# Optimization experiments

Hardware: AMD Instinct MI355X
Metric: run time of the kernel (lower is better)

The kernel has to match this reference:

```python
import jax, jax.numpy as jnp
import numpy as np

S = 14
B = 2
C = 20
LAMBDA_COORD = 5.0
LAMBDA_NOOBJ = 0.5
BATCH = 4096


def setup_inputs() -> dict:
    key = jax.random.key(0)
    k1, k2, k3 = jax.random.split(key, 3)
    pred = jax.random.uniform(k1, (BATCH, S, S, B * 5 + C), dtype=jnp.float32)
    target = jax.random.uniform(k2, (BATCH, S, S, B * 5 + C), dtype=jnp.float32)
    obj = (jax.random.uniform(k3, (BATCH, S, S), dtype=jnp.float32) < 0.15).astype(jnp.float32)
    target = target.at[..., 4].set(obj)
    target = target.at[..., 9].set(obj)
    return {"pred": pred, "target": target}


def _iou(box1, box2):
    # box1, box2: (..., 4) = [x, y, w, h]; elementwise IoU over leading dims
    b1x1 = box1[..., 0] - box1[..., 2] / 2
    b1y1 = box1[..., 1] - box1[..., 3] / 2
    b1x2 = box1[..., 0] + box1[..., 2] / 2
    b1y2 = box1[..., 1] + box1[..., 3] / 2
    b2x1 = box2[..., 0] - box2[..., 2] / 2
    b2y1 = box2[..., 1] - box2[..., 3] / 2
    b2x2 = box2[..., 0] + box2[..., 2] / 2
    b2y2 = box2[..., 1] + box2[..., 3] / 2
    iw = jnp.clip(jnp.minimum(b1x2, b2x2) - jnp.maximum(b1x1, b2x1), 0)
    ih = jnp.clip(jnp.minimum(b1y2, b2y2) - jnp.maximum(b1y1, b2y1), 0)
    inter = iw * ih
    a1 = (b1x2 - b1x1) * (b1y2 - b1y1)
    a2 = (b2x2 - b2x1) * (b2y2 - b2y1)
    return inter / (a1 + a2 - inter + 1e-6)


def reference(pred, target):
    bs = pred.shape[0]
    tb = target[..., : B * 5].reshape(bs, S, S, B, 5)
    pb = pred[..., : B * 5].reshape(bs, S, S, B, 5)
    tcls = target[..., B * 5 :]
    pcls = pred[..., B * 5 :]

    obj_mask = tb[..., 4] > 0          # (bs,S,S,B)
    has_obj = obj_mask[..., 0]         # (bs,S,S)
    noobj_mask = ~obj_mask

    # no-object confidence loss over every non-obj box slot
    conf_err2 = (pb[..., 4] - tb[..., 4]) ** 2
    noobj_loss = jnp.sum(jnp.where(noobj_mask, conf_err2, 0.0))

    # per-box IoU between i-th pred box and i-th target box in each cell
    ious = _iou(pb[..., :4], tb[..., :4])            # (bs,S,S,B)
    best_idx = jnp.argmax(ious, axis=-1)             # (bs,S,S)
    idx = best_idx[..., None, None]
    p_best = jnp.take_along_axis(pb, idx, axis=3)[..., 0, :]  # (bs,S,S,5)
    t_best = jnp.take_along_axis(tb, idx, axis=3)[..., 0, :]

    m = has_obj                                       # (bs,S,S) bool
    mf = m.astype(pred.dtype)

    xy_loss = jnp.sum(mf[..., None] * (p_best[..., :2] - t_best[..., :2]) ** 2)
    p_wh = jnp.sqrt(jnp.abs(p_best[..., 2:4]) + 1e-6)
    t_wh_safe = jnp.where(m[..., None], t_best[..., 2:4], 1.0)  # avoid sqrt(0) grad NaN
    t_wh = jnp.sqrt(t_wh_safe)
    wh_loss = jnp.sum(mf[..., None] * (p_wh - t_wh) ** 2)
    coord_loss = xy_loss + wh_loss

    obj_loss = jnp.sum(mf * (p_best[..., 4] - t_best[..., 4]) ** 2)

    # non-best box confidence pushed to 0 (B=2: the other slot)
    nonbest_conf = jnp.sum(pb[..., 4], axis=-1) - p_best[..., 4]
    noobj_loss = noobj_loss + LAMBDA_NOOBJ * jnp.sum(mf * nonbest_conf ** 2)

    class_loss = jnp.sum(mf[..., None] * (pcls - tcls) ** 2)

    total = LAMBDA_COORD * coord_loss + obj_loss + LAMBDA_NOOBJ * noobj_loss + class_loss
    return total / bs
```

## Files before the change

kernel.cpp:

```cpp
#include <hip/hip_runtime.h>


#define FEAT 30
#define CELLS 802816
#define PAIRS (CELLS / 2)
#define TPB 256
#define NB (PAIRS / TPB)

__device__ __forceinline__ float iou_f(float x1, float y1, float w1, float h1,
                                       float x2, float y2, float w2, float h2) {
    float b1x1 = x1 - 0.5f * w1, b1x2 = x1 + 0.5f * w1;
    float b1y1 = y1 - 0.5f * h1, b1y2 = y1 + 0.5f * h1;
    float b2x1 = x2 - 0.5f * w2, b2x2 = x2 + 0.5f * w2;
    float b2y1 = y2 - 0.5f * h2, b2y2 = y2 + 0.5f * h2;
    float iw = fmaxf(fminf(b1x2, b2x2) - fmaxf(b1x1, b2x1), 0.0f);
    float ih = fmaxf(fminf(b1y2, b2y2) - fmaxf(b1y1, b2y1), 0.0f);
    float inter = iw * ih;
    float a1 = (b1x2 - b1x1) * (b1y2 - b1y1);
    float a2 = (b2x2 - b2x1) * (b2y2 - b2y1);
    return inter / (a1 + a2 - inter + 1e-6f);
}

__device__ __forceinline__ float cell_loss(const float* p, const float* t) {
    const bool obj0 = t[4] > 0.0f;
    const bool obj1 = t[9] > 0.0f;
    const float mf = obj0 ? 1.0f : 0.0f;

    float d0 = p[4] - t[4];
    float d1 = p[9] - t[9];
    float noobj = (obj0 ? 0.0f : d0 * d0) + (obj1 ? 0.0f : d1 * d1);

    float iou0 = iou_f(p[0], p[1], p[2], p[3], t[0], t[1], t[2], t[3]);
    float iou1 = iou_f(p[5], p[6], p[7], p[8], t[5], t[6], t[7], t[8]);
    const bool sel1 = iou1 > iou0;

    float pbx = sel1 ? p[5] : p[0];
    float pby = sel1 ? p[6] : p[1];
    float pbw = sel1 ? p[7] : p[2];
    float pbh = sel1 ? p[8] : p[3];
    float pbc = sel1 ? p[9] : p[4];
    float tbx = sel1 ? t[5] : t[0];
    float tby = sel1 ? t[6] : t[1];
    float tbw = sel1 ? t[7] : t[2];
    float tbh = sel1 ? t[8] : t[3];
    float tbc = sel1 ? t[9] : t[4];

    float dx = pbx - tbx, dy = pby - tby;
    float xy = dx * dx + dy * dy;

    float pw = sqrtf(fabsf(pbw) + 1e-6f);
    float ph = sqrtf(fabsf(pbh) + 1e-6f);
    float tw = sqrtf(obj0 ? tbw : 1.0f);
    float th = sqrtf(obj0 ? tbh : 1.0f);
    float dw = pw - tw, dh = ph - th;
    float wh = dw * dw + dh * dh;

    float dc = pbc - tbc;
    float obj_l = dc * dc;

    float nonbest = (p[4] + p[9]) - pbc;
    noobj += 0.5f * mf * nonbest * nonbest;

    float cls = 0.0f;
#pragma unroll
    for (int k = 10; k < FEAT; ++k) {
        float d = p[k] - t[k];
        cls += d * d;
    }

    return 5.0f * mf * (xy + wh) + mf * obj_l + 0.5f * noobj + mf * cls;
}

__global__ __launch_bounds__(TPB) void yolo_kernel(
        const float* __restrict__ pred, const float* __restrict__ tgt,
        float* __restrict__ out) {
    __shared__ float wave_sum[TPB / 64];

    const int tid = threadIdx.x;
    const long long pair = (long long)blockIdx.x * TPB + tid;

    const float4* gp = (const float4*)(pred + pair * (2 * FEAT));
    const float4* gt = (const float4*)(tgt + pair * (2 * FEAT));

    float pf[2 * FEAT], tf[2 * FEAT];
#pragma unroll
    for (int i = 0; i < 15; ++i) {
        float4 a = gp[i];
        pf[4 * i] = a.x; pf[4 * i + 1] = a.y; pf[4 * i + 2] = a.z; pf[4 * i + 3] = a.w;
        float4 b = gt[i];
        tf[4 * i] = b.x; tf[4 * i + 1] = b.y; tf[4 * i + 2] = b.z; tf[4 * i + 3] = b.w;
    }

    float v = cell_loss(pf, tf) + cell_loss(pf + FEAT, tf + FEAT);

#pragma unroll
    for (int off = 32; off > 0; off >>= 1) v += __shfl_down(v, off, 64);
    if ((tid & 63) == 0) wave_sum[tid >> 6] = v;
    __syncthreads();
    if (tid == 0) {
        float blk = wave_sum[0] + wave_sum[1] + wave_sum[2] + wave_sum[3];
        atomicAdd(out, blk * (1.0f / 4096.0f));
    }
}

extern "C" void kernel_launch(void* const* d_in, const int* in_sizes, int n_in,
                              void* d_out, int out_size, void* d_ws, size_t ws_size,
                              hipStream_t stream) {
    const float* pred = (const float*)d_in[0];
    const float* tgt  = (const float*)d_in[1];
    float* out = (float*)d_out;

    hipMemsetAsync(out, 0, sizeof(float), stream);
    yolo_kernel<<<NB, TPB, 0, stream>>>(pred, tgt, out);
}
```

Measured before the change: 233.3 us.

## Stage cell tiles into LDS with double-buffered global_load_lds in single-wave blocks

Replaces the per-thread strided float4 loads of two cells with coalesced async global-to-LDS copies of 64-cell tiles. Each single-wave block processes eight tiles, prefetching the next tile while computing the current one, then reads each cell from LDS. The aim is fully coalesced DRAM access and overlap of loads with compute. The costs are about 30 KB of LDS per 64-thread block, which limits resident waves per CU, possible LDS bank conflicts from the 30-float stride, and reliance on compiler-inserted waits for the async copies.

```diff
diff --git a/kernel.cpp b/kernel.cpp
--- a/kernel.cpp
+++ b/kernel.cpp
@@ -3,9 +3,17 @@
 
 #define FEAT 30
 #define CELLS 802816
-#define PAIRS (CELLS / 2)
-#define TPB 256
-#define NB (PAIRS / TPB)
+#define TILE_CELLS 64
+#define TILE_FLOATS (TILE_CELLS * FEAT)
+#define BUF_FLOATS (2 * TILE_FLOATS)
+#define TILES_PER_BLOCK 8
+#define NB (CELLS / (TILE_CELLS * TILES_PER_BLOCK))
+
+__device__ __forceinline__ void load16(const float* g, float* l) {
+    __builtin_amdgcn_global_load_lds(
+        (const __attribute__((address_space(1))) void*)g,
+        (__attribute__((address_space(3))) void*)l, 16, 0, 0);
+}
 
 __device__ __forceinline__ float iou_f(float x1, float y1, float w1, float h1,
                                        float x2, float y2, float w2, float h2) {
@@ -71,36 +79,54 @@
     return 5.0f * mf * (xy + wh) + mf * obj_l + 0.5f * noobj + mf * cls;
 }
 
-__global__ __launch_bounds__(TPB) void yolo_kernel(
+__global__ __launch_bounds__(64, 2) void yolo_kernel(
         const float* __restrict__ pred, const float* __restrict__ tgt,
         float* __restrict__ out) {
-    __shared__ float wave_sum[TPB / 64];
+    __shared__ float lds[2 * BUF_FLOATS];
 
-    const int tid = threadIdx.x;
-    const long long pair = (long long)blockIdx.x * TPB + tid;
+    const int lane = threadIdx.x;
+    const float* predT = pred + (long long)blockIdx.x * TILES_PER_BLOCK * TILE_FLOATS;
+    const float* tgtT  = tgt  + (long long)blockIdx.x * TILES_PER_BLOCK * TILE_FLOATS;
 
-    const float4* gp = (const float4*)(pred + pair * (2 * FEAT));
-    const float4* gt = (const float4*)(tgt + pair * (2 * FEAT));
+    const float* pl = predT + lane * 4;
+    const float* ml = (lane < 32) ? (predT + 1792 + lane * 4)
+                                  : (tgtT - 128 + lane * 4);
+    const float* tl = tgtT + 128 + lane * 4;
 
-    float pf[2 * FEAT], tf[2 * FEAT];
+    auto stage = [&](int buf, int tileFloatOff) {
+        float* L = lds + buf * BUF_FLOATS;
+        const float* p = pl + tileFloatOff;
+        const float* m = ml + tileFloatOff;
+        const float* t = tl + tileFloatOff;
 #pragma unroll
-    for (int i = 0; i < 15; ++i) {
-        float4 a = gp[i];
-        pf[4 * i] = a.x; pf[4 * i + 1] = a.y; pf[4 * i + 2] = a.z; pf[4 * i + 3] = a.w;
-        float4 b = gt[i];
-        tf[4 * i] = b.x; tf[4 * i + 1] = b.y; tf[4 * i + 2] = b.z; tf[4 * i + 3] = b.w;
+        for (int j = 0; j < 7; ++j) load16(p + j * 256, L + j * 256);
+        load16(m, L + 1792);
+#pragma unroll
+        for (int j = 0; j < 7; ++j) load16(t + j * 256, L + 2048 + j * 256);
+    };
+
+    stage(0, 0);
+    float acc = 0.0f;
+
+#pragma unroll 1
+    for (int i = 0; i < TILES_PER_BLOCK; ++i) {
+        if (i + 1 < TILES_PER_BLOCK) stage((i + 1) & 1, (i + 1) * TILE_FLOATS);
+
+        const float2* pc = (const float2*)(lds + (i & 1) * BUF_FLOATS + lane * FEAT);
+        const float2* tc = (const float2*)(lds + (i & 1) * BUF_FLOATS + TILE_FLOATS + lane * FEAT);
+        float pf[FEAT], tf[FEAT];
+#pragma unroll
+        for (int k = 0; k < FEAT / 2; ++k) {
+            float2 a = pc[k]; pf[2 * k] = a.x; pf[2 * k + 1] = a.y;
+            float2 b = tc[k]; tf[2 * k] = b.x; tf[2 * k + 1] = b.y;
+        }
+        acc += cell_loss(pf, tf);
     }
 
-    float v = cell_loss(pf, tf) + cell_loss(pf + FEAT, tf + FEAT);
-
+    float v = acc;
 #pragma unroll
     for (int off = 32; off > 0; off >>= 1) v += __shfl_down(v, off, 64);
-    if ((tid & 63) == 0) wave_sum[tid >> 6] = v;
-    __syncthreads();
-    if (tid == 0) {
-        float blk = wave_sum[0] + wave_sum[1] + wave_sum[2] + wave_sum[3];
-        atomicAdd(out, blk * (1.0f / 4096.0f));
-    }
+    if (lane == 0) atomicAdd(out, v * (1.0f / 4096.0f));
 }
 
 extern "C" void kernel_launch(void* const* d_in, const int* in_sizes, int n_in,
@@ -111,5 +137,5 @@
     float* out = (float*)d_out;
 
     hipMemsetAsync(out, 0, sizeof(float), stream);
-    yolo_kernel<<<NB, TPB, 0, stream>>>(pred, tgt, out);
+    yolo_kernel<<<NB, 64, 0, stream>>>(pred, tgt, out);
 }
```

Result: faster. 215.2 us (-7.8%).
